# Optimization experiments

Hardware: AMD Instinct MI355X
Metric: run time of the kernel (lower is better)

## Reference

```python
import jax, jax.numpy as jnp
import numpy as np


def setup_inputs() -> dict:
    key = jax.random.key(0)
    k1, k2 = jax.random.split(key)
    B, L, C, H, W = 1, 16, 8, 128, 128
    # flows scaled so cumulative displacements stay mostly inside [-1, 1]
    flows = jax.random.normal(k1, (B, L, 2, H, W), jnp.float32) * 0.1
    images = jax.random.normal(k2, (B, L, C, H, W), jnp.float32)
    return {"flows": flows, "images": images}


def _base_grid(H, W, dtype):
    step_y, step_x = 2.0 / H, 2.0 / W
    gy = jnp.linspace(-1.0 + step_y * 0.5, 1.0 - step_y * 0.5, H, dtype=dtype)
    gx = jnp.linspace(-1.0 + step_x * 0.5, 1.0 - step_x * 0.5, W, dtype=dtype)
    mx, my = jnp.meshgrid(gx, gy, indexing="xy")  # each [H, W]
    return jnp.stack([mx, my], axis=-1)  # [H, W, 2], (x, y)


def _grid_sample_bilinear(img, grid):
    # img: [C, H, W]; grid: [H, W, 2] normalized coords in [-1, 1]
    # matches torch grid_sample(mode='bilinear', padding_mode='zeros', align_corners=False)
    C, H, W = img.shape
    ix = (grid[..., 0] + 1.0) * (W * 0.5) - 0.5
    iy = (grid[..., 1] + 1.0) * (H * 0.5) - 0.5
    x0 = jnp.floor(ix)
    y0 = jnp.floor(iy)
    wx = ix - x0
    wy = iy - y0

    def gather(xf, yf):
        xi = xf.astype(jnp.int32)
        yi = yf.astype(jnp.int32)
        valid = ((xf >= 0) & (xf < W) & (yf >= 0) & (yf < H)).astype(img.dtype)
        xi = jnp.clip(xi, 0, W - 1)
        yi = jnp.clip(yi, 0, H - 1)
        return img[:, yi, xi] * valid  # [C, H, W]

    return (
        gather(x0, y0) * ((1.0 - wx) * (1.0 - wy))
        + gather(x0 + 1.0, y0) * (wx * (1.0 - wy))
        + gather(x0, y0 + 1.0) * ((1.0 - wx) * wy)
        + gather(x0 + 1.0, y0 + 1.0) * (wx * wy)
    )


def reference(flows, images):
    B, L, C, H, W = images.shape
    dtype = flows.dtype
    cum = jnp.cumsum(flows.astype(jnp.float32), axis=1).astype(dtype)  # [B,L,2,H,W]
    base = _base_grid(H, W, dtype)  # [H,W,2]

    # pairwise relative flow: rel[b,t,k] = cum[b,t] - cum[b,k]  -> [B,L,L,2,H,W]
    rel = cum[:, :, None] - cum[:, None, :]
    grid = base + jnp.transpose(rel, (0, 1, 2, 4, 5, 3))  # [B,L,L,H,W,2]
    gx = jnp.remainder(grid[..., 0] + 1.0, 2.0) - 1.0  # wrap x periodically
    grid = jnp.concatenate([gx[..., None], grid[..., 1:]], axis=-1)

    # sample images[b,k] at grid[b,t,k]
    sample_k = jax.vmap(_grid_sample_bilinear, in_axes=(0, 0))       # over k
    sample_tk = jax.vmap(sample_k, in_axes=(None, 0))                # over t
    sample_btk = jax.vmap(sample_tk, in_axes=(0, 0))                 # over b
    sampled = sample_btk(images, grid)  # [B,L,L,C,H,W]

    # triangular accumulation: out[b,t] = sum_{k<=t} sampled[b,t,k]
    mask = jnp.tril(jnp.ones((L, L), dtype=dtype))
    return jnp.einsum("btkchw,tk->btchw", sampled, mask)
```

## Files before the change

### kernel.cpp

```cpp
#include <hip/hip_runtime.h>
#include <hip/hip_fp16.h>

constexpr int L = 16, C = 8, H = 128, W = 128;
constexpr int HW = H * W;

__global__ __launch_bounds__(256) void prep_k(const float* __restrict__ flows,
                                              const float* __restrict__ images,
                                              float* __restrict__ cum,
                                              __half* __restrict__ timg) {
    int b = blockIdx.x;
    constexpr int TB = (L * HW) / 256;
    if (b < TB) {
        int idx = b * 256 + threadIdx.x;
        int l = idx >> 14, pix = idx & (HW - 1);
        const float* src = images + (size_t)l * C * HW + pix;
        float4 packed;
        __half2* hp = reinterpret_cast<__half2*>(&packed);
        hp[0] = __floats2half2_rn(src[0 * HW], src[1 * HW]);
        hp[1] = __floats2half2_rn(src[2 * HW], src[3 * HW]);
        hp[2] = __floats2half2_rn(src[4 * HW], src[5 * HW]);
        hp[3] = __floats2half2_rn(src[6 * HW], src[7 * HW]);
        reinterpret_cast<float4*>(timg)[idx] = packed;
    } else {
        int idx = (b - TB) * 256 + threadIdx.x;
        int comp = idx >> 14, pix = idx & (HW - 1);
        const float* src = flows + comp * HW + pix;
        float* dst = cum + comp * HW + pix;
        float s = 0.f;
#pragma unroll
        for (int l = 0; l < L; ++l) {
            s += src[(size_t)l * 2 * HW];
            dst[(size_t)l * 2 * HW] = s;
        }
    }
}

__device__ __forceinline__ void samp(float acc[8], float relx, float rely,
                                     float bx1, float by1,
                                     const __half* __restrict__ img) {
    float xr = bx1 + relx;
    xr = fmaf(-2.0f, floorf(xr * 0.5f), xr);
    float yr = by1 + rely;
    float ix = xr * (W * 0.5f) - 0.5f;
    float iy = yr * (H * 0.5f) - 0.5f;
    float x0f = floorf(ix), y0f = floorf(iy);
    float wx = ix - x0f, wy = iy - y0f;
#pragma unroll
    for (int dy = 0; dy < 2; ++dy) {
#pragma unroll
        for (int dx = 0; dx < 2; ++dx) {
            float xf = x0f + (float)dx;
            float yf = y0f + (float)dy;
            bool valid = (xf >= 0.f) & (xf < (float)W) & (yf >= 0.f) & (yf < (float)H);
            float wgt = (dx ? wx : 1.f - wx) * (dy ? wy : 1.f - wy);
            wgt = valid ? wgt : 0.f;
            int xi = (int)xf; xi = xi < 0 ? 0 : (xi > W - 1 ? W - 1 : xi);
            int yi = (int)yf; yi = yi < 0 ? 0 : (yi > H - 1 ? H - 1 : yi);
            float4 raw = *reinterpret_cast<const float4*>(img + (yi * W + xi) * C);
            const __half* hv = reinterpret_cast<const __half*>(&raw);
#pragma unroll
            for (int c = 0; c < 8; ++c)
                acc[c] = fmaf(__half2float(hv[c]), wgt, acc[c]);
        }
    }
}

constexpr int TPB = 128;
__global__ __launch_bounds__(TPB) void sample_k(const float* __restrict__ cum,
                                                const __half* __restrict__ timg,
                                                float* __restrict__ out) {
    int p   = blockIdx.x >> 7;
    int pix = (blockIdx.x & 127) * TPB + threadIdx.x;
    int h = pix >> 7, w = pix & (W - 1);
    float bx1 = (w + 0.5f) * (2.0f / W);
    float by1 = (h + 0.5f) * (2.0f / H);

    int t1 = p, t2 = 15 - p;
    float c1x = cum[(size_t)(2 * t1)     * HW + pix];
    float c1y = cum[(size_t)(2 * t1 + 1) * HW + pix];
    float c2x = cum[(size_t)(2 * t2)     * HW + pix];
    float c2y = cum[(size_t)(2 * t2 + 1) * HW + pix];

    float acc1[8] = {0, 0, 0, 0, 0, 0, 0, 0};
    float acc2[8] = {0, 0, 0, 0, 0, 0, 0, 0};

    for (int k = 0; k <= t2; ++k) {
        float ckx = cum[(size_t)(2 * k)     * HW + pix];
        float cky = cum[(size_t)(2 * k + 1) * HW + pix];
        const __half* img = timg + (size_t)k * HW * C;
        samp(acc2, c2x - ckx, c2y - cky, bx1, by1, img);
        if (k <= t1)
            samp(acc1, c1x - ckx, c1y - cky, bx1, by1, img);
    }

    size_t o1 = (size_t)t1 * C * HW + pix;
    size_t o2 = (size_t)t2 * C * HW + pix;
#pragma unroll
    for (int c = 0; c < 8; ++c) {
        out[o1 + c * HW] = acc1[c];
        out[o2 + c * HW] = acc2[c];
    }
}

extern "C" void kernel_launch(void* const* d_in, const int* in_sizes, int n_in,
                              void* d_out, int out_size, void* d_ws, size_t ws_size,
                              hipStream_t stream) {
    const float* flows  = (const float*)d_in[0];
    const float* images = (const float*)d_in[1];
    float* out = (float*)d_out;

    float*  cum  = (float*)d_ws;
    __half* timg = (__half*)((char*)d_ws + (size_t)2 * L * HW * sizeof(float));

    prep_k<<<(L * HW) / 256 + (2 * HW) / 256, 256, 0, stream>>>(flows, images, cum, timg);
    sample_k<<<8 * (HW / TPB), TPB, 0, stream>>>(cum, timg, out);
}
```

Baseline: 85.58 us.

## Use nontemporal loads/stores, simplify bilinear weights, and double sample block size

Marks the streaming image and flow reads and the output writes as nontemporal so they do not pollute cache. The bilinear sampler now computes separable x/y validity weights and clamped indices once, issues four float4 gathers up front, and combines the corners with a chained fma per channel. The sampling kernel moves from 128 to 256 threads per block, which halves the block count to 512 and may reduce occupancy flexibility.

```diff
diff --git a/kernel.cpp b/kernel.cpp
--- a/kernel.cpp
+++ b/kernel.cpp
@@ -3,6 +3,7 @@
 
 constexpr int L = 16, C = 8, H = 128, W = 128;
 constexpr int HW = H * W;
+constexpr int CHW = C * HW;
 
 __global__ __launch_bounds__(256) void prep_k(const float* __restrict__ flows,
                                               const float* __restrict__ images,
@@ -13,13 +14,21 @@
     if (b < TB) {
         int idx = b * 256 + threadIdx.x;
         int l = idx >> 14, pix = idx & (HW - 1);
-        const float* src = images + (size_t)l * C * HW + pix;
+        const float* src = images + (size_t)l * CHW + pix;
+        float v0 = __builtin_nontemporal_load(src + 0 * HW);
+        float v1 = __builtin_nontemporal_load(src + 1 * HW);
+        float v2 = __builtin_nontemporal_load(src + 2 * HW);
+        float v3 = __builtin_nontemporal_load(src + 3 * HW);
+        float v4 = __builtin_nontemporal_load(src + 4 * HW);
+        float v5 = __builtin_nontemporal_load(src + 5 * HW);
+        float v6 = __builtin_nontemporal_load(src + 6 * HW);
+        float v7 = __builtin_nontemporal_load(src + 7 * HW);
         float4 packed;
         __half2* hp = reinterpret_cast<__half2*>(&packed);
-        hp[0] = __floats2half2_rn(src[0 * HW], src[1 * HW]);
-        hp[1] = __floats2half2_rn(src[2 * HW], src[3 * HW]);
-        hp[2] = __floats2half2_rn(src[4 * HW], src[5 * HW]);
-        hp[3] = __floats2half2_rn(src[6 * HW], src[7 * HW]);
+        hp[0] = __floats2half2_rn(v0, v1);
+        hp[1] = __floats2half2_rn(v2, v3);
+        hp[2] = __floats2half2_rn(v4, v5);
+        hp[3] = __floats2half2_rn(v6, v7);
         reinterpret_cast<float4*>(timg)[idx] = packed;
     } else {
         int idx = (b - TB) * 256 + threadIdx.x;
@@ -29,7 +38,7 @@
         float s = 0.f;
 #pragma unroll
         for (int l = 0; l < L; ++l) {
-            s += src[(size_t)l * 2 * HW];
+            s += __builtin_nontemporal_load(src + (size_t)l * 2 * HW);
             dst[(size_t)l * 2 * HW] = s;
         }
     }
@@ -41,36 +50,45 @@
     float xr = bx1 + relx;
     xr = fmaf(-2.0f, floorf(xr * 0.5f), xr);
     float yr = by1 + rely;
-    float ix = xr * (W * 0.5f) - 0.5f;
-    float iy = yr * (H * 0.5f) - 0.5f;
+    float ix = fmaf(xr, W * 0.5f, -0.5f);
+    float iy = fmaf(yr, H * 0.5f, -0.5f);
     float x0f = floorf(ix), y0f = floorf(iy);
     float wx = ix - x0f, wy = iy - y0f;
+    int x0 = (int)x0f, y0 = (int)y0f;
+
+    float wx0 = ((unsigned)x0       < (unsigned)W) ? 1.f - wx : 0.f;
+    float wx1 = ((unsigned)(x0 + 1) < (unsigned)W) ? wx       : 0.f;
+    float wy0 = ((unsigned)y0       < (unsigned)H) ? 1.f - wy : 0.f;
+    float wy1 = ((unsigned)(y0 + 1) < (unsigned)H) ? wy       : 0.f;
+    int xi0 = min(max(x0, 0), W - 1), xi1 = min(max(x0 + 1, 0), W - 1);
+    int yi0 = min(max(y0, 0), H - 1), yi1 = min(max(y0 + 1, 0), H - 1);
+
+    const float4* p = reinterpret_cast<const float4*>(img);
+    float4 r00 = p[yi0 * W + xi0];
+    float4 r01 = p[yi0 * W + xi1];
+    float4 r10 = p[yi1 * W + xi0];
+    float4 r11 = p[yi1 * W + xi1];
+    float w00 = wx0 * wy0, w01 = wx1 * wy0, w10 = wx0 * wy1, w11 = wx1 * wy1;
+    const __half* h00 = reinterpret_cast<const __half*>(&r00);
+    const __half* h01 = reinterpret_cast<const __half*>(&r01);
+    const __half* h10 = reinterpret_cast<const __half*>(&r10);
+    const __half* h11 = reinterpret_cast<const __half*>(&r11);
 #pragma unroll
-    for (int dy = 0; dy < 2; ++dy) {
-#pragma unroll
-        for (int dx = 0; dx < 2; ++dx) {
-            float xf = x0f + (float)dx;
-            float yf = y0f + (float)dy;
-            bool valid = (xf >= 0.f) & (xf < (float)W) & (yf >= 0.f) & (yf < (float)H);
-            float wgt = (dx ? wx : 1.f - wx) * (dy ? wy : 1.f - wy);
-            wgt = valid ? wgt : 0.f;
-            int xi = (int)xf; xi = xi < 0 ? 0 : (xi > W - 1 ? W - 1 : xi);
-            int yi = (int)yf; yi = yi < 0 ? 0 : (yi > H - 1 ? H - 1 : yi);
-            float4 raw = *reinterpret_cast<const float4*>(img + (yi * W + xi) * C);
-            const __half* hv = reinterpret_cast<const __half*>(&raw);
-#pragma unroll
-            for (int c = 0; c < 8; ++c)
-                acc[c] = fmaf(__half2float(hv[c]), wgt, acc[c]);
-        }
+    for (int c = 0; c < 8; ++c) {
+        float v = fmaf(__half2float(h00[c]), w00,
+                  fmaf(__half2float(h01[c]), w01,
+                  fmaf(__half2float(h10[c]), w10,
+                       __half2float(h11[c]) * w11)));
+        acc[c] += v;
     }
 }
 
-constexpr int TPB = 128;
+constexpr int TPB = 256;
 __global__ __launch_bounds__(TPB) void sample_k(const float* __restrict__ cum,
                                                 const __half* __restrict__ timg,
                                                 float* __restrict__ out) {
-    int p   = blockIdx.x >> 7;
-    int pix = (blockIdx.x & 127) * TPB + threadIdx.x;
+    int p   = blockIdx.x >> 6;
+    int pix = (blockIdx.x & 63) * TPB + threadIdx.x;
     int h = pix >> 7, w = pix & (W - 1);
     float bx1 = (w + 0.5f) * (2.0f / W);
     float by1 = (h + 0.5f) * (2.0f / H);
@@ -93,12 +111,12 @@
             samp(acc1, c1x - ckx, c1y - cky, bx1, by1, img);
     }
 
-    size_t o1 = (size_t)t1 * C * HW + pix;
-    size_t o2 = (size_t)t2 * C * HW + pix;
+    size_t o1 = (size_t)t1 * CHW + pix;
+    size_t o2 = (size_t)t2 * CHW + pix;
 #pragma unroll
     for (int c = 0; c < 8; ++c) {
-        out[o1 + c * HW] = acc1[c];
-        out[o2 + c * HW] = acc2[c];
+        __builtin_nontemporal_store(acc1[c], out + o1 + (size_t)c * HW);
+        __builtin_nontemporal_store(acc2[c], out + o2 + (size_t)c * HW);
     }
 }
 
@@ -110,7 +128,7 @@
     float* out = (float*)d_out;
 
     float*  cum  = (float*)d_ws;
-    __half* timg = (__half*)((char*)d_ws + (size_t)2 * L * HW * sizeof(float));
+    __half* timg = (__half*)((char*)d_ws + (size_t)2 * L * HW * 4);
 
     prep_k<<<(L * HW) / 256 + (2 * HW) / 256, 256, 0, stream>>>(flows, images, cum, timg);
     sample_k<<<8 * (HW / TPB), TPB, 0, stream>>>(cum, timg, out);
```

New measurement: 88.57 us. +3.5%, slower.
